# Kernel tuning notes

Measured on AMD Instinct MI355X. Metric: run time of the kernel, lower is better.

The kernel has to match this reference:

```python
import jax, jax.numpy as jnp
import numpy as np

B, D, E, H, C = 16384, 512, 16, 2048, 1
LN_EPS = 1e-5


def setup_inputs() -> dict:
    key = jax.random.key(0)
    ks = jax.random.split(key, 6)
    scale = 0.02
    return {
        "z": jax.random.normal(ks[0], (B, D), jnp.float32),
        "gate_w": jax.random.normal(ks[1], (D, E), jnp.float32) * scale,
        "gate_b": jnp.zeros((E,), jnp.float32),
        "ln_scale": jnp.ones((E, D), jnp.float32),
        "ln_bias": jnp.zeros((E, D), jnp.float32),
        "w1": jax.random.normal(ks[2], (E, D, H), jnp.float32) * scale,
        "b1": jnp.zeros((E, H), jnp.float32),
        "w2": jax.random.normal(ks[3], (E, H, C), jnp.float32) * scale,
        "b2": jnp.zeros((E, C), jnp.float32),
    }


def reference(z, gate_w, gate_b, ln_scale, ln_bias, w1, b1, w2, b2):
    # Gate: softmax over experts, top-1 routing by argmax
    g = jax.nn.softmax(z @ gate_w + gate_b, axis=-1)  # (B, E)
    idx = jnp.argmax(g, axis=-1)                      # (B,)

    # LayerNorm statistics are expert-independent (affine differs per expert)
    mu = jnp.mean(z, axis=-1, keepdims=True)
    var = jnp.mean(jnp.square(z - mu), axis=-1, keepdims=True)
    zn = (z - mu) / jnp.sqrt(var + LN_EPS)            # (B, D)

    # Loop over the small fixed expert set; combine by top-1 mask.
    logits = jnp.zeros((z.shape[0],), z.dtype)
    for e in range(E):
        x = zn * ln_scale[e] + ln_bias[e]                       # (B, D)
        h = jax.nn.gelu(x @ w1[e] + b1[e], approximate=False)   # (B, H)
        o = jnp.squeeze(h @ w2[e] + b2[e], axis=-1)             # (B,) since C==1
        logits = jnp.where(idx == e, o, logits)
    return logits, g
```

## Files before the change

kernel.cpp:

```cpp
#include <hip/hip_runtime.h>
#include <math.h>

#define NB 16384
#define ND 512
#define NE 16
#define NH 2048
#define BM 128
#define BN 128
#define BK 64
#define NCH (NH / BN)
#define NTB 4
#define NPW (NCH * 2)
#define LN_EPS 1e-5f

typedef __attribute__((ext_vector_type(8))) short s8v;
typedef __attribute__((ext_vector_type(4))) float f4v;

#define WS_W1T_OFF   ((size_t)0)
#define WS_W1T_BYTES ((size_t)NE * NH * ND * 2)
#define WS_XN_OFF    (WS_W1T_OFF + WS_W1T_BYTES)
#define WS_XN_BYTES  ((size_t)NB * ND * 2)
#define WS_XNS_OFF   (WS_XN_OFF + WS_XN_BYTES)
#define WS_XNS_BYTES ((size_t)NB * ND * 2)
#define WS_PART_OFF  (WS_XNS_OFF + WS_XNS_BYTES)
#define WS_PART_BYTES ((size_t)NB * NPW * 4)
#define WS_IDX_OFF   (WS_PART_OFF + WS_PART_BYTES)
#define WS_ROWOF_OFF (WS_IDX_OFF + (size_t)NB * 4)
#define WS_CNT_OFF   (WS_ROWOF_OFF + (size_t)NB * 4)
#define WS_ROWS_OFF  (WS_CNT_OFF + 256)

__device__ __forceinline__ unsigned short bf16_rne(float f) {
    unsigned u = __float_as_uint(f);
    unsigned r = (u + 0x7fffu + ((u >> 16) & 1u)) >> 16;
    return (unsigned short)r;
}

__global__ __launch_bounds__(256) void w1conv_kernel(
    const float* __restrict__ w1, unsigned short* __restrict__ w1t)
{
    int bid = blockIdx.x;
    int e = bid & 15;
    int rest = bid >> 4;
    int db = rest & 7;
    int hb = rest >> 3;
    int h = hb * 256 + threadIdx.x;

    const float* src = w1 + ((size_t)e * ND + db * 64) * NH + h;
    unsigned int u[32];
#pragma unroll
    for (int p = 0; p < 32; ++p) {
        float f0 = src[(size_t)(2 * p) * NH];
        float f1 = src[(size_t)(2 * p + 1) * NH];
        u[p] = (unsigned)bf16_rne(f0) | ((unsigned)bf16_rne(f1) << 16);
    }
    uint4* dst = reinterpret_cast<uint4*>(
        w1t + ((size_t)e * NH + h) * ND + db * 64);
#pragma unroll
    for (int p = 0; p < 8; ++p)
        dst[p] = make_uint4(u[4 * p], u[4 * p + 1], u[4 * p + 2], u[4 * p + 3]);
}

__global__ __launch_bounds__(256) void gate_ln_kernel(
    const float* __restrict__ z, const float* __restrict__ gw,
    const float* __restrict__ gb, const float* __restrict__ ln_s,
    const float* __restrict__ ln_b, unsigned short* __restrict__ xn,
    int* __restrict__ idx_ws, float* __restrict__ g_out)
{
    int wave = threadIdx.x >> 6;
    int lane = threadIdx.x & 63;
    int b = blockIdx.x * 4 + wave;
    int q = lane & 3, dg = lane >> 2;

    const float* zr = z + (size_t)b * ND;
    float4 zv[8];
#pragma unroll
    for (int i = 0; i < 8; ++i)
        zv[i] = *reinterpret_cast<const float4*>(zr + dg * 32 + i * 4);

    float sum = 0.f, ssq = 0.f;
    float ga[4] = {0.f, 0.f, 0.f, 0.f};
#pragma unroll
    for (int i = 0; i < 8; ++i) {
        float zs[4] = {zv[i].x, zv[i].y, zv[i].z, zv[i].w};
#pragma unroll
        for (int t = 0; t < 4; ++t) {
            int d = dg * 32 + i * 4 + t;
            float4 w4 = *reinterpret_cast<const float4*>(gw + (size_t)d * NE + q * 4);
            ga[0] = fmaf(zs[t], w4.x, ga[0]);
            ga[1] = fmaf(zs[t], w4.y, ga[1]);
            ga[2] = fmaf(zs[t], w4.z, ga[2]);
            ga[3] = fmaf(zs[t], w4.w, ga[3]);
            sum += zs[t];
            ssq = fmaf(zs[t], zs[t], ssq);
        }
    }
#pragma unroll
    for (int m = 4; m <= 32; m <<= 1) {
        sum += __shfl_xor(sum, m);
        ssq += __shfl_xor(ssq, m);
#pragma unroll
        for (int j = 0; j < 4; ++j) ga[j] += __shfl_xor(ga[j], m);
    }
#pragma unroll
    for (int j = 0; j < 4; ++j) ga[j] += gb[q * 4 + j];

    float mu = sum * (1.f / ND);
    float var = ssq * (1.f / ND) - mu * mu;
    float rstd = rsqrtf(var + LN_EPS);

    float lmax = fmaxf(fmaxf(ga[0], ga[1]), fmaxf(ga[2], ga[3]));
    lmax = fmaxf(lmax, __shfl_xor(lmax, 1));
    lmax = fmaxf(lmax, __shfl_xor(lmax, 2));
    float ge[4], lsum = 0.f;
#pragma unroll
    for (int j = 0; j < 4; ++j) { ge[j] = __expf(ga[j] - lmax); lsum += ge[j]; }
    lsum += __shfl_xor(lsum, 1);
    lsum += __shfl_xor(lsum, 2);
    float rden = 1.f / lsum;

    int li = 1000;
#pragma unroll
    for (int j = 3; j >= 0; --j) if (ga[j] == lmax) li = q * 4 + j;
    li = min(li, __shfl_xor(li, 1));
    li = min(li, __shfl_xor(li, 2));

    float gv0 = ge[0] * rden, gv1 = ge[1] * rden;
    float gv2 = ge[2] * rden, gv3 = ge[3] * rden;
    int srcl = lane >> 2;
    float t0 = __shfl(gv0, srcl), t1 = __shfl(gv1, srcl);
    float t2 = __shfl(gv2, srcl), t3 = __shfl(gv3, srcl);
    float gval = (q == 0) ? t0 : (q == 1) ? t1 : (q == 2) ? t2 : t3;
    if (lane < NE) g_out[(size_t)b * NE + lane] = gval;

    float4 xa, xc;
    if (q == 0)      { xa = zv[0]; xc = zv[1]; }
    else if (q == 1) { xa = zv[2]; xc = zv[3]; }
    else if (q == 2) { xa = zv[4]; xc = zv[5]; }
    else             { xa = zv[6]; xc = zv[7]; }
    int dofs = dg * 32 + q * 8;
    const float* ls = ln_s + (size_t)li * ND + dofs;
    const float* lb = ln_b + (size_t)li * ND + dofs;
    float4 s0 = *reinterpret_cast<const float4*>(ls);
    float4 s1 = *reinterpret_cast<const float4*>(ls + 4);
    float4 u0 = *reinterpret_cast<const float4*>(lb);
    float4 u1 = *reinterpret_cast<const float4*>(lb + 4);
    unsigned short xb[8];
    xb[0] = bf16_rne((xa.x - mu) * rstd * s0.x + u0.x);
    xb[1] = bf16_rne((xa.y - mu) * rstd * s0.y + u0.y);
    xb[2] = bf16_rne((xa.z - mu) * rstd * s0.z + u0.z);
    xb[3] = bf16_rne((xa.w - mu) * rstd * s0.w + u0.w);
    xb[4] = bf16_rne((xc.x - mu) * rstd * s1.x + u1.x);
    xb[5] = bf16_rne((xc.y - mu) * rstd * s1.y + u1.y);
    xb[6] = bf16_rne((xc.z - mu) * rstd * s1.z + u1.z);
    xb[7] = bf16_rne((xc.w - mu) * rstd * s1.w + u1.w);
    *reinterpret_cast<s8v*>(xn + (size_t)b * ND + dofs) =
        *reinterpret_cast<s8v*>(xb);

    if (lane == 0) idx_ws[b] = li;
}

__global__ __launch_bounds__(256) void bucket_kernel(
    const int* __restrict__ idx_ws, int* __restrict__ counts,
    int* __restrict__ rows)
{
    __shared__ int qc[4];
    int e = blockIdx.x;
    int tid = threadIdx.x, w = tid >> 6, lane = tid & 63;
    const int4* p = reinterpret_cast<const int4*>(idx_ws) + (size_t)w * 1024;

    int c = 0;
#pragma unroll 4
    for (int it = 0; it < 16; ++it) {
        int4 v = p[it * 64 + lane];
        c += (v.x == e) + (v.y == e) + (v.z == e) + (v.w == e);
    }
#pragma unroll
    for (int m = 1; m < 64; m <<= 1) c += __shfl_xor(c, m);
    if (lane == 0) qc[w] = c;
    __syncthreads();

    int base = 0;
    for (int j = 0; j < w; ++j) base += qc[j];
    unsigned long long below = (lane == 0) ? 0ull : ((~0ull) >> (64 - lane));
    int* re = rows + (size_t)e * NB;
    int run = base;
#pragma unroll 2
    for (int it = 0; it < 16; ++it) {
        int4 v = p[it * 64 + lane];
        int vv[4] = {v.x, v.y, v.z, v.w};
#pragma unroll
        for (int k = 0; k < 4; ++k) {
            unsigned long long m = __ballot(vv[k] == e);
            if (vv[k] == e)
                re[run + __popcll(m & below)] = w * 4096 + (it * 64 + lane) * 4 + k;
            run += __popcll(m);
        }
    }
    if (tid == 0) counts[e] = qc[0] + qc[1] + qc[2] + qc[3];
}

__global__ __launch_bounds__(256) void gather_kernel(
    const unsigned short* __restrict__ xn, const int* __restrict__ counts,
    const int* __restrict__ rows, unsigned short* __restrict__ xns,
    int* __restrict__ rowof)
{
    int wave = threadIdx.x >> 6, lane = threadIdx.x & 63;
    int slot = blockIdx.x * 4 + wave;

    int pfx = 0, e = 0;
#pragma unroll
    for (int i = 0; i < NE; ++i) {
        int c = counts[i];
        if (e == i && slot >= pfx + c) { pfx += c; e = i + 1; }
    }
    int row = rows[(size_t)e * NB + (slot - pfx)];
    s8v v = *reinterpret_cast<const s8v*>(xn + (size_t)row * ND + lane * 8);
    *reinterpret_cast<s8v*>(xns + (size_t)slot * ND + lane * 8) = v;
    if (lane == 0) rowof[slot] = row;
}

__global__ __launch_bounds__(256, 2) void mfma_mlp(
    const unsigned short* __restrict__ xns, const unsigned short* __restrict__ w1t,
    const float* __restrict__ b1, const float* __restrict__ w2,
    const int* __restrict__ counts, float* __restrict__ part)
{
    __shared__ unsigned short A_lds[BM * BK];
    __shared__ unsigned short B_lds[BN * BK];

    int bid = blockIdx.x;
    int e = bid & 15;
    int rest = bid >> 4;
    int ch = rest & 15;
    int tb0 = rest >> 4;
    int c0 = ch * BN;
    int tid = threadIdx.x, lane = tid & 63, wave = tid >> 6;
    int wm = wave & 1, wn = wave >> 1;

    int cnt = counts[e];
    int pfx = 0;
    for (int i = 0; i < e; ++i) pfx += counts[i];

    int rquad = lane >> 3;
    int sbyte = ((lane & 7) * 16) ^ (rquad << 4);

    size_t boff[4];
#pragma unroll
    for (int i = 0; i < 4; ++i) {
        int cl = (wave * 4 + i) * 8 + rquad;
        boff[i] = ((size_t)(e * NH + c0 + cl) * ND) * 2 + sbyte;
    }

    float b1v[4], w2v[4];
#pragma unroll
    for (int cf = 0; cf < 4; ++cf) {
        int col = c0 + wn * 64 + cf * 16 + (lane & 15);
        b1v[cf] = b1[(size_t)e * NH + col];
        w2v[cf] = w2[(size_t)e * NH + col];
    }

    int g = lane >> 4;
    int fr = lane & 15;
    int sw = (lane & 7) << 4;
    int aoffs[4], boffs[4];
#pragma unroll
    for (int f = 0; f < 4; ++f) {
        aoffs[f] = (wm * 64 + f * 16 + fr) * 128;
        boffs[f] = (wn * 64 + f * 16 + fr) * 128;
    }

    for (int tb = tb0; tb * BM < cnt; tb += NTB) {
        int rbase = tb * BM;
        int sbase = pfx + rbase;

        f4v acc[4][4];
#pragma unroll
        for (int rf = 0; rf < 4; ++rf)
#pragma unroll
            for (int cf = 0; cf < 4; ++cf) acc[rf][cf] = (f4v){0.f, 0.f, 0.f, 0.f};

#pragma unroll
        for (int ss = 0; ss < 8; ++ss) {
            __syncthreads();
#pragma unroll
            for (int i = 0; i < 4; ++i) {
                int rloc = (wave * 4 + i) * 8 + rquad;
                int slot = min(sbase + rloc, NB - 1);
                __builtin_amdgcn_global_load_lds(
                    (const __attribute__((address_space(1))) void*)
                        ((const char*)xns + (size_t)slot * 1024 + ss * 128 + sbyte),
                    (__attribute__((address_space(3))) void*)
                        &A_lds[(wave * 4 + i) * 8 * BK], 16, 0, 0);
                __builtin_amdgcn_global_load_lds(
                    (const __attribute__((address_space(1))) void*)
                        ((const char*)w1t + boff[i] + ss * 128),
                    (__attribute__((address_space(3))) void*)
                        &B_lds[(wave * 4 + i) * 8 * BK], 16, 0, 0);
            }
            __syncthreads();

#pragma unroll
            for (int ks = 0; ks < 2; ++ks) {
                int kb = (ks * 64 + g * 16) ^ sw;
                s8v a[4], bb[4];
#pragma unroll
                for (int rf = 0; rf < 4; ++rf)
                    a[rf] = *reinterpret_cast<const s8v*>(
                        (const char*)A_lds + aoffs[rf] + kb);
#pragma unroll
                for (int cf = 0; cf < 4; ++cf)
                    bb[cf] = *reinterpret_cast<const s8v*>(
                        (const char*)B_lds + boffs[cf] + kb);
#pragma unroll
                for (int rf = 0; rf < 4; ++rf)
#pragma unroll
                    for (int cf = 0; cf < 4; ++cf)
                        acc[rf][cf] = __builtin_amdgcn_mfma_f32_16x16x32_bf16(
                            a[rf], bb[cf], acc[rf][cf], 0, 0, 0);
            }
        }

#pragma unroll
        for (int rf = 0; rf < 4; ++rf) {
            float pj[4] = {0.f, 0.f, 0.f, 0.f};
#pragma unroll
            for (int cf = 0; cf < 4; ++cf) {
#pragma unroll
                for (int j = 0; j < 4; ++j) {
                    float h = acc[rf][cf][j] + b1v[cf];
                    float uu = h * (0.7978845608f + 0.0356774081f * h * h);
                    float ex = __expf(2.f * uu);
                    float th = 1.f - 2.f / (ex + 1.f);
                    pj[j] = fmaf(0.5f * h * (1.f + th), w2v[cf], pj[j]);
                }
            }
#pragma unroll
            for (int m = 1; m < 16; m <<= 1)
#pragma unroll
                for (int j = 0; j < 4; ++j) pj[j] += __shfl_xor(pj[j], m);
            if ((lane & 15) == 0) {
#pragma unroll
                for (int j = 0; j < 4; ++j) {
                    int rloc = wm * 64 + rf * 16 + g * 4 + j;
                    if (rbase + rloc < cnt)
                        part[(size_t)(sbase + rloc) * NPW + ch * 2 + wn] = pj[j];
                }
            }
        }
    }
}

__global__ __launch_bounds__(256) void finalize_kernel(
    const float* __restrict__ part, const int* __restrict__ rowof,
    const int* __restrict__ idx_ws, const float* __restrict__ b2,
    float* __restrict__ logits)
{
    int s = blockIdx.x * 256 + threadIdx.x;
    const f4v* p = reinterpret_cast<const f4v*>(part + (size_t)s * NPW);
    float sum = 0.f;
#pragma unroll
    for (int i = 0; i < 8; ++i) {
        f4v v = p[i];
        sum += (v[0] + v[1]) + (v[2] + v[3]);
    }
    int row = rowof[s];
    logits[row] = sum + b2[idx_ws[row]];
}

extern "C" void kernel_launch(void* const* d_in, const int* in_sizes, int n_in,
                              void* d_out, int out_size, void* d_ws, size_t ws_size,
                              hipStream_t stream) {
    const float* z    = (const float*)d_in[0];
    const float* gw   = (const float*)d_in[1];
    const float* gb   = (const float*)d_in[2];
    const float* ln_s = (const float*)d_in[3];
    const float* ln_b = (const float*)d_in[4];
    const float* w1   = (const float*)d_in[5];
    const float* b1   = (const float*)d_in[6];
    const float* w2   = (const float*)d_in[7];
    const float* b2   = (const float*)d_in[8];

    float* logits = (float*)d_out;
    float* g_out  = (float*)d_out + NB;

    char* ws = (char*)d_ws;
    unsigned short* w1t = (unsigned short*)(ws + WS_W1T_OFF);
    unsigned short* xn  = (unsigned short*)(ws + WS_XN_OFF);
    unsigned short* xns = (unsigned short*)(ws + WS_XNS_OFF);
    float* part  = (float*)(ws + WS_PART_OFF);
    int* idx_ws  = (int*)(ws + WS_IDX_OFF);
    int* rowof   = (int*)(ws + WS_ROWOF_OFF);
    int* cnts    = (int*)(ws + WS_CNT_OFF);
    int* rowl    = (int*)(ws + WS_ROWS_OFF);

    w1conv_kernel<<<NE * 64, 256, 0, stream>>>(w1, w1t);
    gate_ln_kernel<<<NB / 4, 256, 0, stream>>>(z, gw, gb, ln_s, ln_b,
                                               xn, idx_ws, g_out);
    bucket_kernel<<<NE, 256, 0, stream>>>(idx_ws, cnts, rowl);
    gather_kernel<<<NB / 4, 256, 0, stream>>>(xn, cnts, rowl, xns, rowof);
    mfma_mlp<<<NE * NCH * NTB, 256, 0, stream>>>(xns, w1t, b1, w2, cnts, part);
    finalize_kernel<<<NB / 256, 256, 0, stream>>>(part, rowof, idx_ws, b2,
                                                  logits);
}
```

Before: 144.3 us.

## Enlarge MLP GEMM tiles, double-buffer LDS loads, and use persistent grid

Raises the expert GEMM tile to 256x256 with 8 waves, double-buffers the A/B LDS stages so global-to-LDS loads for the next K slice overlap MFMA work, and switches to a fixed 512-block persistent grid that strides over (expert, row tile, column chunk) units. It also raises wave priority around the MFMA section. The aim is more reuse per loaded byte and hidden load latency, at the cost of 128KB LDS per block and higher register pressure, which may limit occupancy and worsen load balance for small experts.

```diff
diff --git a/kernel.cpp b/kernel.cpp
--- a/kernel.cpp
+++ b/kernel.cpp
@@ -5,12 +5,13 @@
 #define ND 512
 #define NE 16
 #define NH 2048
-#define BM 128
-#define BN 128
+#define BM 256
+#define BN 256
 #define BK 64
-#define NCH (NH / BN)
-#define NTB 4
-#define NPW (NCH * 2)
+#define NCHU 8
+#define NPW 32
+#define UCAP (NE * 64 * NCHU)
+#define GEMM_GRID 512
 #define LN_EPS 1e-5f
 
 typedef __attribute__((ext_vector_type(8))) short s8v;
@@ -219,23 +220,19 @@
     if (lane == 0) rowof[slot] = row;
 }
 
-__global__ __launch_bounds__(256, 2) void mfma_mlp(
+__global__ __launch_bounds__(512, 2) void mfma_mlp(
     const unsigned short* __restrict__ xns, const unsigned short* __restrict__ w1t,
     const float* __restrict__ b1, const float* __restrict__ w2,
     const int* __restrict__ counts, float* __restrict__ part)
 {
-    __shared__ unsigned short A_lds[BM * BK];
-    __shared__ unsigned short B_lds[BN * BK];
+    __shared__ unsigned short A_lds[2][BM * BK];
+    __shared__ unsigned short B_lds[2][BN * BK];
 
     int bid = blockIdx.x;
-    int e = bid & 15;
-    int rest = bid >> 4;
-    int ch = rest & 15;
-    int tb0 = rest >> 4;
-    int c0 = ch * BN;
     int tid = threadIdx.x, lane = tid & 63, wave = tid >> 6;
     int wm = wave & 1, wn = wave >> 1;
 
+    int e = bid & 15;
     int cnt = counts[e];
     int pfx = 0;
     for (int i = 0; i < e; ++i) pfx += counts[i];
@@ -243,84 +240,96 @@
     int rquad = lane >> 3;
     int sbyte = ((lane & 7) * 16) ^ (rquad << 4);
 
-    size_t boff[4];
-#pragma unroll
-    for (int i = 0; i < 4; ++i) {
-        int cl = (wave * 4 + i) * 8 + rquad;
-        boff[i] = ((size_t)(e * NH + c0 + cl) * ND) * 2 + sbyte;
-    }
-
-    float b1v[4], w2v[4];
-#pragma unroll
-    for (int cf = 0; cf < 4; ++cf) {
-        int col = c0 + wn * 64 + cf * 16 + (lane & 15);
-        b1v[cf] = b1[(size_t)e * NH + col];
-        w2v[cf] = w2[(size_t)e * NH + col];
-    }
-
     int g = lane >> 4;
     int fr = lane & 15;
     int sw = (lane & 7) << 4;
-    int aoffs[4], boffs[4];
-#pragma unroll
-    for (int f = 0; f < 4; ++f) {
-        aoffs[f] = (wm * 64 + f * 16 + fr) * 128;
-        boffs[f] = (wn * 64 + f * 16 + fr) * 128;
-    }
-
-    for (int tb = tb0; tb * BM < cnt; tb += NTB) {
-        int rbase = tb * BM;
+    int aoffs[8], boffs[4];
+#pragma unroll
+    for (int f = 0; f < 8; ++f) aoffs[f] = (wm * 128 + f * 16 + fr) * 128;
+#pragma unroll
+    for (int f = 0; f < 4; ++f) boffs[f] = (wn * 64 + f * 16 + fr) * 128;
+
+    size_t ebase = (size_t)e * NH;
+
+#define ISSUE_AB(buf, sbase, c0, ss)                                         \
+    {   _Pragma("unroll")                                                    \
+        for (int i = 0; i < 4; ++i) {                                        \
+            int rloc = wave * 32 + i * 8 + rquad;                            \
+            int slot = min((sbase) + rloc, NB - 1);                          \
+            __builtin_amdgcn_global_load_lds(                                \
+                (const __attribute__((address_space(1))) void*)              \
+                    ((const char*)xns + (size_t)slot * 1024 + (ss) * 128 + sbyte), \
+                (__attribute__((address_space(3))) void*)                    \
+                    &A_lds[buf][(wave * 32 + i * 8) * BK], 16, 0, 0);        \
+            __builtin_amdgcn_global_load_lds(                                \
+                (const __attribute__((address_space(1))) void*)              \
+                    ((const char*)w1t + (ebase + (c0) + rloc) * 1024 + (ss) * 128 + sbyte), \
+                (__attribute__((address_space(3))) void*)                    \
+                    &B_lds[buf][(wave * 32 + i * 8) * BK], 16, 0, 0); } }
+
+    for (int u = bid; u < UCAP; u += GEMM_GRID) {
+        int rest = u >> 4;
+        int rt = rest >> 3;
+        int ch = rest & 7;
+        int rbase = rt * BM;
+        if (rbase >= cnt) continue;
         int sbase = pfx + rbase;
-
-        f4v acc[4][4];
-#pragma unroll
-        for (int rf = 0; rf < 4; ++rf)
+        int c0 = ch * BN;
+
+        float b1v[4], w2v[4];
+#pragma unroll
+        for (int cf = 0; cf < 4; ++cf) {
+            int col = c0 + wn * 64 + cf * 16 + fr;
+            b1v[cf] = b1[ebase + col];
+            w2v[cf] = w2[ebase + col];
+        }
+
+        f4v acc[8][4];
+#pragma unroll
+        for (int rf = 0; rf < 8; ++rf)
 #pragma unroll
             for (int cf = 0; cf < 4; ++cf) acc[rf][cf] = (f4v){0.f, 0.f, 0.f, 0.f};
 
+        ISSUE_AB(0, sbase, c0, 0);
+
 #pragma unroll
         for (int ss = 0; ss < 8; ++ss) {
-            __syncthreads();
-#pragma unroll
-            for (int i = 0; i < 4; ++i) {
-                int rloc = (wave * 4 + i) * 8 + rquad;
-                int slot = min(sbase + rloc, NB - 1);
-                __builtin_amdgcn_global_load_lds(
-                    (const __attribute__((address_space(1))) void*)
-                        ((const char*)xns + (size_t)slot * 1024 + ss * 128 + sbyte),
-                    (__attribute__((address_space(3))) void*)
-                        &A_lds[(wave * 4 + i) * 8 * BK], 16, 0, 0);
-                __builtin_amdgcn_global_load_lds(
-                    (const __attribute__((address_space(1))) void*)
-                        ((const char*)w1t + boff[i] + ss * 128),
-                    (__attribute__((address_space(3))) void*)
-                        &B_lds[(wave * 4 + i) * 8 * BK], 16, 0, 0);
+            int cb = ss & 1;
+            __builtin_amdgcn_s_barrier();
+            if (ss < 7) {
+                ISSUE_AB(cb ^ 1, sbase, c0, ss + 1);
+                asm volatile("s_waitcnt vmcnt(8)" ::: "memory");
+            } else {
+                asm volatile("s_waitcnt vmcnt(0)" ::: "memory");
             }
-            __syncthreads();
-
+            __builtin_amdgcn_s_barrier();
+            __builtin_amdgcn_sched_barrier(0);
+
+            __builtin_amdgcn_s_setprio(1);
 #pragma unroll
             for (int ks = 0; ks < 2; ++ks) {
                 int kb = (ks * 64 + g * 16) ^ sw;
-                s8v a[4], bb[4];
-#pragma unroll
-                for (int rf = 0; rf < 4; ++rf)
+                s8v a[8], bb[4];
+#pragma unroll
+                for (int rf = 0; rf < 8; ++rf)
                     a[rf] = *reinterpret_cast<const s8v*>(
-                        (const char*)A_lds + aoffs[rf] + kb);
+                        (const char*)&A_lds[cb][0] + aoffs[rf] + kb);
 #pragma unroll
                 for (int cf = 0; cf < 4; ++cf)
                     bb[cf] = *reinterpret_cast<const s8v*>(
-                        (const char*)B_lds + boffs[cf] + kb);
-#pragma unroll
-                for (int rf = 0; rf < 4; ++rf)
+                        (const char*)&B_lds[cb][0] + boffs[cf] + kb);
+#pragma unroll
+                for (int rf = 0; rf < 8; ++rf)
 #pragma unroll
                     for (int cf = 0; cf < 4; ++cf)
                         acc[rf][cf] = __builtin_amdgcn_mfma_f32_16x16x32_bf16(
                             a[rf], bb[cf], acc[rf][cf], 0, 0, 0);
             }
+            __builtin_amdgcn_s_setprio(0);
         }
 
 #pragma unroll
-        for (int rf = 0; rf < 4; ++rf) {
+        for (int rf = 0; rf < 8; ++rf) {
             float pj[4] = {0.f, 0.f, 0.f, 0.f};
 #pragma unroll
             for (int cf = 0; cf < 4; ++cf) {
@@ -340,13 +349,14 @@
             if ((lane & 15) == 0) {
 #pragma unroll
                 for (int j = 0; j < 4; ++j) {
-                    int rloc = wm * 64 + rf * 16 + g * 4 + j;
+                    int rloc = wm * 128 + rf * 16 + g * 4 + j;
                     if (rbase + rloc < cnt)
-                        part[(size_t)(sbase + rloc) * NPW + ch * 2 + wn] = pj[j];
+                        part[(size_t)(sbase + rloc) * NPW + ch * 4 + wn] = pj[j];
                 }
             }
         }
     }
+#undef ISSUE_AB
 }
 
 __global__ __launch_bounds__(256) void finalize_kernel(
@@ -397,7 +407,7 @@
                                                xn, idx_ws, g_out);
     bucket_kernel<<<NE, 256, 0, stream>>>(idx_ws, cnts, rowl);
     gather_kernel<<<NB / 4, 256, 0, stream>>>(xn, cnts, rowl, xns, rowof);
-    mfma_mlp<<<NE * NCH * NTB, 256, 0, stream>>>(xns, w1t, b1, w2, cnts, part);
+    mfma_mlp<<<GEMM_GRID, 512, 0, stream>>>(xns, w1t, b1, w2, cnts, part);
     finalize_kernel<<<NB / 256, 256, 0, stream>>>(part, rowof, idx_ws, b2,
                                                   logits);
 }
```

After: 159.9 us. 1.11x slower.
